# Performance work log

Hardware: AMD Instinct MI355X
Metric: run time of the kernel (lower is better)

## Reference

```python
import jax, jax.numpy as jnp
import numpy as np
import math

DIM = 1024
NUM_HEADS = 16
HEAD_DIM = DIM // NUM_HEADS  # 64
BATCH = 4
SEQ = 4096


def setup_inputs() -> dict:
    key = jax.random.key(0)
    ks = jax.random.split(key, 10)
    s = 1.0 / math.sqrt(DIM)
    return {
        "x": jax.random.normal(ks[0], (BATCH, SEQ, DIM), dtype=jnp.float32),
        "Wq": jax.random.normal(ks[1], (DIM, DIM), dtype=jnp.float32) * s,
        "bq": jax.random.normal(ks[2], (DIM,), dtype=jnp.float32) * 0.01,
        "Wk": jax.random.normal(ks[3], (DIM, DIM), dtype=jnp.float32) * s,
        "bk": jax.random.normal(ks[4], (DIM,), dtype=jnp.float32) * 0.01,
        "Wv": jax.random.normal(ks[5], (DIM, DIM), dtype=jnp.float32) * s,
        "bv": jax.random.normal(ks[6], (DIM,), dtype=jnp.float32) * 0.01,
        "Wo": jax.random.normal(ks[7], (DIM, DIM), dtype=jnp.float32) * s,
        "bo": jax.random.normal(ks[8], (DIM,), dtype=jnp.float32) * 0.01,
        # Performer random projection buffer: randn * 0.4, [head_dim, feature_map_size]
        "R": jax.random.normal(ks[9], (HEAD_DIM, HEAD_DIM), dtype=jnp.float32) * 0.4,
    }


def _feature_map(x, R):
    # x: [b, h, n, d]; matches torch: x scaled first, then norm of scaled x
    x = x / math.sqrt(HEAD_DIM)
    proj = jnp.einsum("bhnd,dm->bhnm", x, R)
    sq_norm = jnp.sum(x * x, axis=-1, keepdims=True)  # ||x||^2
    return jnp.exp(proj - 0.5 * sq_norm)


def reference(x, Wq, bq, Wk, bk, Wv, bv, Wo, bo, R):
    b, n, _ = x.shape
    h, d = NUM_HEADS, HEAD_DIM

    def split_heads(t):
        return t.reshape(b, n, h, d).transpose(0, 2, 1, 3)  # [b,h,n,d]

    q = split_heads(x @ Wq.T + bq)
    k = split_heads(x @ Wk.T + bk)
    v = split_heads(x @ Wv.T + bv)

    q_prime = _feature_map(q, R)  # [b,h,n,m]
    k_prime = _feature_map(k, R)  # [b,h,n,m]

    kv = jnp.einsum("bhnd,bhne->bhde", k_prime, v)          # [b,h,m,d]
    z = 1.0 / (jnp.sum(q_prime, axis=-1) + 1e-8)            # [b,h,n]
    out = jnp.einsum("bhnd,bhde,bhn->bhne", q_prime, kv, z)  # [b,h,n,d]

    out = out.transpose(0, 2, 1, 3).reshape(b, n, DIM)
    return out @ Wo.T + bo
```

## Files before the change

### kernel.cpp

```cpp
#include <hip/hip_runtime.h>
#include <math.h>

#define DIM 1024
#define NH 16
#define HD 64
#define BATCH 4
#define SEQ 4096
#define NTOK (BATCH*SEQ)

typedef float f32x4 __attribute__((ext_vector_type(4)));
typedef short bf16x8 __attribute__((ext_vector_type(8)));

#define GLOAD_LDS16(gp, lp)                                                    \
  __builtin_amdgcn_global_load_lds(                                            \
      (const __attribute__((address_space(1))) unsigned int*)(gp),             \
      (__attribute__((address_space(3))) unsigned int*)(lp), 16, 0, 0)

__device__ __forceinline__ unsigned short f2bf(float f) {
  unsigned u = __float_as_uint(f);
  unsigned r = (u + 0x7fffu + ((u >> 16) & 1u)) >> 16;
  return (unsigned short)r;
}
__device__ __forceinline__ float bf2f(unsigned short s) {
  return __uint_as_float((unsigned)s << 16);
}

template <int NT_N, int OUT_BF16>
__global__ __launch_bounds__(512, 2) void gemm256(
    const unsigned short* __restrict__ A,
    const unsigned short* __restrict__ B,
    const float* __restrict__ b0, const float* __restrict__ b1,
    const float* __restrict__ b2,
    void* __restrict__ C0, void* __restrict__ C1, void* __restrict__ C2)
{
    __shared__ unsigned short SA[4][8192];
    __shared__ unsigned short SB[4][8192];
    const int t    = threadIdx.x;
    const int lane = t & 63;
    const int w    = t >> 6;

    const int cpx = gridDim.x >> 3;
    const int swz = (blockIdx.x & 7) * cpx + (blockIdx.x >> 3);
    const int mi  = swz / NT_N;
    const int ni  = swz % NT_N;
    const int m0  = mi * 256;
    const int n0g = ni * 256;

    const int wm = (w >> 2) * 128;
    const int wn = (w & 3) * 64;

    const int srow = t >> 2;
    const int sseg = ((t & 3) ^ ((t >> 3) & 3)) * 8;
    const unsigned short* Ag = A + (size_t)(m0 + srow) * 1024 + sseg;
    const unsigned short* Bg = B + (size_t)(n0g + srow) * 1024 + sseg;
    const int ldst = w * 512;

    const int fr = lane & 15;
    const int fq = ((lane >> 4) ^ ((fr >> 1) & 3)) * 8;

    const unsigned abase = (unsigned)(size_t)
        (__attribute__((address_space(3))) unsigned short*)&SA[0][0]
        + (unsigned)(((wm + fr) * 32 + fq) * 2);
    const unsigned bbase = (unsigned)(size_t)
        (__attribute__((address_space(3))) unsigned short*)&SB[0][0]
        + (unsigned)(((wn + fr) * 32 + fq) * 2);

    f32x4 acc[8][4] = {};
    bf16x8 a1[4], a2[4], bb[2][4];

#define STGA(k, j)                                                            \
  GLOAD_LDS16(Ag + (size_t)(j) * 131072 + (size_t)(k) * 32,                   \
              &SA[(k) & 3][(j) * 4096 + ldst])
#define STGB(k, j)                                                            \
  GLOAD_LDS16(Bg + (size_t)(j) * 131072 + (size_t)(k) * 32,                   \
              &SB[(k) & 3][(j) * 4096 + ldst])
#define DSR(dst, base, imm)                                                   \
  asm volatile("ds_read_b128 %0, %1 offset:%2"                                \
               : "=v"(dst) : "v"(base), "i"(imm))
#define VMW_(N) asm volatile("s_waitcnt vmcnt(" #N ")" ::: "memory")
#define VMW(N) VMW_(N)
#define LGKM0                                                                 \
  asm volatile("s_waitcnt lgkmcnt(0)" ::: "memory");                          \
  __builtin_amdgcn_sched_barrier(0)
#define BARRIER                                                               \
  __builtin_amdgcn_s_barrier();                                               \
  __builtin_amdgcn_sched_barrier(0)

#define BODY(h, VM, DOSTG, DORD)                                              \
  {                                                                           \
    LGKM0;                                                                    \
    _Pragma("unroll")                                                         \
    for (int mf = 0; mf < 4; ++mf)                                            \
      DSR(a2[mf], abase, ((h) & 3) * 16384 + 4096 + mf * 1024);               \
    if (DOSTG) {                                                              \
      STGA((h) + 3, 0); STGA((h) + 3, 1);                                     \
      STGB((h) + 3, 0); STGB((h) + 3, 1);                                     \
    }                                                                         \
    __builtin_amdgcn_s_setprio(1);                                            \
    _Pragma("unroll")                                                         \
    for (int mf = 0; mf < 4; ++mf)                                            \
      _Pragma("unroll")                                                       \
      for (int nf = 0; nf < 4; ++nf)                                          \
        acc[mf][nf] = __builtin_amdgcn_mfma_f32_16x16x32_bf16(                \
            a1[mf], bb[(h) & 1][nf], acc[mf][nf], 0, 0, 0);                   \
    __builtin_amdgcn_s_setprio(0);                                            \
    VMW(VM);                                                                  \
    BARRIER;                                                                  \
    LGKM0;                                                                    \
    if (DORD) {                                                               \
      _Pragma("unroll")                                                       \
      for (int nf = 0; nf < 4; ++nf)                                          \
        DSR(bb[((h) + 1) & 1][nf], bbase,                                     \
            (((h) + 1) & 3) * 16384 + nf * 1024);                             \
      _Pragma("unroll")                                                       \
      for (int mf = 0; mf < 4; ++mf)                                          \
        DSR(a1[mf], abase, (((h) + 1) & 3) * 16384 + mf * 1024);              \
    }                                                                         \
    __builtin_amdgcn_s_setprio(1);                                            \
    _Pragma("unroll")                                                         \
    for (int mf = 0; mf < 4; ++mf)                                            \
      _Pragma("unroll")                                                       \
      for (int nf = 0; nf < 4; ++nf)                                          \
        acc[4 + mf][nf] = __builtin_amdgcn_mfma_f32_16x16x32_bf16(            \
            a2[mf], bb[(h) & 1][nf], acc[4 + mf][nf], 0, 0, 0);               \
    __builtin_amdgcn_s_setprio(0);                                            \
    BARRIER;                                                                  \
  }

    STGA(0, 0); STGA(0, 1); STGB(0, 0); STGB(0, 1);
    STGA(1, 0); STGA(1, 1); STGB(1, 0); STGB(1, 1);
    STGA(2, 0); STGA(2, 1); STGB(2, 0); STGB(2, 1);
    VMW(8);
    BARRIER;
#pragma unroll
    for (int nf = 0; nf < 4; ++nf)
        DSR(bb[0][nf], bbase, nf * 1024);
#pragma unroll
    for (int mf = 0; mf < 4; ++mf)
        DSR(a1[mf], abase, mf * 1024);

    BODY(0, 8, 1, 1)  BODY(1, 8, 1, 1)  BODY(2, 8, 1, 1)  BODY(3, 8, 1, 1)
    BODY(4, 8, 1, 1)  BODY(5, 8, 1, 1)  BODY(6, 8, 1, 1)  BODY(7, 8, 1, 1)
    BODY(8, 8, 1, 1)  BODY(9, 8, 1, 1)  BODY(10, 8, 1, 1) BODY(11, 8, 1, 1)
    BODY(12, 8, 1, 1) BODY(13, 8, 1, 1) BODY(14, 8, 1, 1) BODY(15, 8, 1, 1)
    BODY(16, 8, 1, 1) BODY(17, 8, 1, 1) BODY(18, 8, 1, 1) BODY(19, 8, 1, 1)
    BODY(20, 8, 1, 1) BODY(21, 8, 1, 1) BODY(22, 8, 1, 1) BODY(23, 8, 1, 1)
    BODY(24, 8, 1, 1) BODY(25, 8, 1, 1) BODY(26, 8, 1, 1) BODY(27, 8, 1, 1)
    BODY(28, 8, 1, 1) BODY(29, 4, 0, 1) BODY(30, 0, 0, 1) BODY(31, 0, 0, 0)

#undef BODY
#undef BARRIER
#undef LGKM0
#undef VMW
#undef VMW_
#undef DSR
#undef STGB
#undef STGA

    const int mat = ni >> 2;
    const float* bias = (mat == 0) ? b0 : (mat == 1) ? b1 : b2;
    void* Cp = (mat == 0) ? C0 : (mat == 1) ? C1 : C2;
    const int n0 = (ni & 3) * 256;

    const int col = lane & 15;
    const int rq  = (lane >> 4) * 4;
#pragma unroll
    for (int nf = 0; nf < 4; ++nf) {
        int cbase = n0 + wn + nf * 16 + col;
        float bv = bias[cbase];
#pragma unroll
        for (int mf = 0; mf < 8; ++mf) {
            int rbase = m0 + wm + (mf >> 2) * 64 + (mf & 3) * 16 + rq;
#pragma unroll
            for (int r = 0; r < 4; ++r) {
                float val = acc[mf][nf][r] + bv;
                size_t idx = (size_t)(rbase + r) * 1024 + cbase;
                if (OUT_BF16)
                    ((unsigned short*)Cp)[idx] = f2bf(val);
                else
                    ((float*)Cp)[idx] = val;
            }
        }
    }
}

__global__ __launch_bounds__(256) void cast_bf16(
    const float* __restrict__ src, unsigned short* __restrict__ dst, int n)
{
    int i = (blockIdx.x * 256 + threadIdx.x) * 4;
    if (i >= n) return;
    float4 v = *(const float4*)&src[i];
    ushort2 lo = {f2bf(v.x), f2bf(v.y)};
    ushort2 hi = {f2bf(v.z), f2bf(v.w)};
    *(ushort2*)&dst[i] = lo;
    *(ushort2*)&dst[i + 2] = hi;
}

__global__ __launch_bounds__(256) void cast_bf16_w4(
    const float* __restrict__ s0, const float* __restrict__ s1,
    const float* __restrict__ s2, const float* __restrict__ s3,
    unsigned short* __restrict__ d0, unsigned short* __restrict__ d1,
    unsigned short* __restrict__ d2, unsigned short* __restrict__ d3)
{
    const float* s = (blockIdx.y == 0) ? s0 : (blockIdx.y == 1) ? s1
                    : (blockIdx.y == 2) ? s2 : s3;
    unsigned short* d = (blockIdx.y == 0) ? d0 : (blockIdx.y == 1) ? d1
                       : (blockIdx.y == 2) ? d2 : d3;
    int i = (blockIdx.x * 256 + threadIdx.x) * 4;
    float4 v = *(const float4*)&s[i];
    ushort2 lo = {f2bf(v.x), f2bf(v.y)};
    ushort2 hi = {f2bf(v.z), f2bf(v.w)};
    *(ushort2*)&d[i] = lo;
    *(ushort2*)&d[i + 2] = hi;
}

__global__ __launch_bounds__(256) void featmap_mfma(
    unsigned short* __restrict__ buf, const float* __restrict__ R)
{
    __shared__ unsigned short Rt[64 * 72];
    const int t = threadIdx.x;
    for (int i = t; i < 4096; i += 256) {
        int n = i >> 6, k = i & 63;
        Rt[n * 72 + k] = f2bf(R[k * 64 + n]);
    }
    __syncthreads();

    const int lane = t & 63;
    const int w = t >> 6;
    const size_t rowbase = (size_t)blockIdx.x * 256 + w * 64;
    const int fr = lane & 15;
    const int fq = (lane >> 4) * 8;

    f32x4 acc[4][4] = {};
    float sqacc[4] = {0.f, 0.f, 0.f, 0.f};

#pragma unroll
    for (int ks = 0; ks < 2; ks++) {
        bf16x8 bfr[4];
#pragma unroll
        for (int nt = 0; nt < 4; nt++)
            bfr[nt] = *(const bf16x8*)&Rt[(nt * 16 + fr) * 72 + ks * 32 + fq];
#pragma unroll
        for (int mt = 0; mt < 4; mt++) {
            bf16x8 a = *(const bf16x8*)
                &buf[(rowbase + mt * 16 + fr) * 64 + ks * 32 + fq];
#pragma unroll
            for (int j = 0; j < 8; j++) {
                float v = bf2f((unsigned short)a[j]);
                sqacc[mt] = fmaf(v, v, sqacc[mt]);
            }
#pragma unroll
            for (int nt = 0; nt < 4; nt++)
                acc[mt][nt] = __builtin_amdgcn_mfma_f32_16x16x32_bf16(
                    a, bfr[nt], acc[mt][nt], 0, 0, 0);
        }
    }
#pragma unroll
    for (int mt = 0; mt < 4; mt++) {
        sqacc[mt] += __shfl_xor(sqacc[mt], 16);
        sqacc[mt] += __shfl_xor(sqacc[mt], 32);
    }

    const int col = lane & 15;
    const int rq  = (lane >> 4) * 4;
#pragma unroll
    for (int mt = 0; mt < 4; mt++) {
#pragma unroll
        for (int r = 0; r < 4; r++) {
            float s = __shfl(sqacc[mt], rq + r);
            size_t row = rowbase + mt * 16 + rq + r;
#pragma unroll
            for (int nt = 0; nt < 4; nt++) {
                float val = acc[mt][nt][r] * 0.125f - s * 0.0078125f;
                buf[row * 64 + nt * 16 + col] = f2bf(__expf(val));
            }
        }
    }
}

__global__ __launch_bounds__(256) void kv_accum(
    const unsigned short* __restrict__ kp, const unsigned short* __restrict__ vp,
    float* __restrict__ kv)
{
    __shared__ float Ks[16][68];
    __shared__ float Vs[16][68];
    const int chunk = blockIdx.x;
    const int h = blockIdx.y;
    const int b = blockIdx.z;
    const int t = threadIdx.x;
    const int tx = t & 15, ty = t >> 4;
    float c[4][4] = {};
    const int nbase = b * SEQ + chunk * 512;
    const int nl = t >> 4, seg = t & 15;
    for (int n0 = 0; n0 < 512; n0 += 16) {
        size_t gaddr = (size_t)(nbase + n0 + nl) * DIM + h * 64 + seg * 4;
        ushort4 kq = *(const ushort4*)&kp[gaddr];
        ushort4 vq = *(const ushort4*)&vp[gaddr];
        Ks[nl][seg * 4 + 0] = bf2f(kq.x); Ks[nl][seg * 4 + 1] = bf2f(kq.y);
        Ks[nl][seg * 4 + 2] = bf2f(kq.z); Ks[nl][seg * 4 + 3] = bf2f(kq.w);
        Vs[nl][seg * 4 + 0] = bf2f(vq.x); Vs[nl][seg * 4 + 1] = bf2f(vq.y);
        Vs[nl][seg * 4 + 2] = bf2f(vq.z); Vs[nl][seg * 4 + 3] = bf2f(vq.w);
        __syncthreads();
#pragma unroll
        for (int nn = 0; nn < 16; nn++) {
            float4 a = *(const float4*)&Ks[nn][ty * 4];
            float4 bq = *(const float4*)&Vs[nn][tx * 4];
            float aa[4] = {a.x, a.y, a.z, a.w};
            float bb[4] = {bq.x, bq.y, bq.z, bq.w};
#pragma unroll
            for (int i = 0; i < 4; i++)
#pragma unroll
                for (int j = 0; j < 4; j++)
                    c[i][j] += aa[i] * bb[j];
        }
        __syncthreads();
    }
    float* dst = &kv[(size_t)(b * NH + h) * 64 * 64];
#pragma unroll
    for (int i = 0; i < 4; i++)
#pragma unroll
        for (int j = 0; j < 4; j++)
            atomicAdd(&dst[(ty * 4 + i) * 64 + tx * 4 + j], c[i][j]);
}

__global__ __launch_bounds__(256) void attn_out_mfma(
    const unsigned short* __restrict__ qp, const float* __restrict__ kv,
    unsigned short* __restrict__ ob)
{
    __shared__ unsigned short kvT[64 * 72];
    const int t = threadIdx.x;
    const int bh = blockIdx.y;
    const int b = bh >> 4, h = bh & 15;
    const float* kvp = &kv[(size_t)bh * 4096];
    for (int i = t; i < 4096; i += 256) {
        int m = i >> 6, e = i & 63;
        kvT[e * 72 + m] = f2bf(kvp[i]);
    }
    __syncthreads();

    const int lane = t & 63;
    const int w = t >> 6;
    const int rowInSeq = blockIdx.x * 256 + w * 64;
    const int fr = lane & 15;
    const int fq = (lane >> 4) * 8;

    f32x4 acc[4][4] = {};
    float rsum[4] = {0.f, 0.f, 0.f, 0.f};

#pragma unroll
    for (int ks = 0; ks < 2; ks++) {
        bf16x8 bfr[4];
#pragma unroll
        for (int nt = 0; nt < 4; nt++)
            bfr[nt] = *(const bf16x8*)&kvT[(nt * 16 + fr) * 72 + ks * 32 + fq];
#pragma unroll
        for (int mt = 0; mt < 4; mt++) {
            size_t n = (size_t)(b * SEQ + rowInSeq + mt * 16 + fr);
            bf16x8 a = *(const bf16x8*)&qp[n * DIM + h * 64 + ks * 32 + fq];
#pragma unroll
            for (int j = 0; j < 8; j++)
                rsum[mt] += bf2f((unsigned short)a[j]);
#pragma unroll
            for (int nt = 0; nt < 4; nt++)
                acc[mt][nt] = __builtin_amdgcn_mfma_f32_16x16x32_bf16(
                    a, bfr[nt], acc[mt][nt], 0, 0, 0);
        }
    }
#pragma unroll
    for (int mt = 0; mt < 4; mt++) {
        rsum[mt] += __shfl_xor(rsum[mt], 16);
        rsum[mt] += __shfl_xor(rsum[mt], 32);
    }

    const int col = lane & 15;
    const int rq  = (lane >> 4) * 4;
#pragma unroll
    for (int mt = 0; mt < 4; mt++) {
#pragma unroll
        for (int r = 0; r < 4; r++) {
            float s = __shfl(rsum[mt], rq + r);
            float z = 1.f / (s + 1e-8f);
            size_t n = (size_t)(b * SEQ + rowInSeq + mt * 16 + rq + r);
#pragma unroll
            for (int nt = 0; nt < 4; nt++)
                ob[n * DIM + h * 64 + nt * 16 + col] = f2bf(acc[mt][nt][r] * z);
        }
    }
}

extern "C" void kernel_launch(void* const* d_in, const int* in_sizes, int n_in,
                              void* d_out, int out_size, void* d_ws, size_t ws_size,
                              hipStream_t stream) {
    const float* x  = (const float*)d_in[0];
    const float* Wq = (const float*)d_in[1];
    const float* bq = (const float*)d_in[2];
    const float* Wk = (const float*)d_in[3];
    const float* bk = (const float*)d_in[4];
    const float* Wv = (const float*)d_in[5];
    const float* bv = (const float*)d_in[6];
    const float* Wo = (const float*)d_in[7];
    const float* bo = (const float*)d_in[8];
    const float* R  = (const float*)d_in[9];
    float* out = (float*)d_out;

    char* p = (char*)d_ws;
    unsigned short* xb = (unsigned short*)p; p += (size_t)NTOK * DIM * 2;
    unsigned short* qb = (unsigned short*)p; p += (size_t)NTOK * DIM * 2;
    unsigned short* kb = (unsigned short*)p; p += (size_t)NTOK * DIM * 2;
    unsigned short* vb = (unsigned short*)p; p += (size_t)NTOK * DIM * 2;
    float* kvb = (float*)p;                  p += (size_t)BATCH * NH * HD * HD * 4;
    unsigned short* wqkv = (unsigned short*)p; p += (size_t)3 * DIM * DIM * 2;
    unsigned short* wob  = (unsigned short*)p; p += (size_t)DIM * DIM * 2;

    hipMemsetAsync(kvb, 0, (size_t)BATCH * NH * HD * HD * sizeof(float), stream);

    cast_bf16<<<NTOK * DIM / (256 * 4), 256, 0, stream>>>(x, xb, NTOK * DIM);
    cast_bf16_w4<<<dim3(DIM * DIM / (256 * 4), 4), 256, 0, stream>>>(
        Wq, Wk, Wv, Wo,
        wqkv, wqkv + (size_t)DIM * DIM, wqkv + (size_t)2 * DIM * DIM, wob);

    gemm256<12, 1><<<768, 512, 0, stream>>>(
        xb, wqkv, bq, bk, bv, qb, kb, vb);

    featmap_mfma<<<2 * NTOK * NH / 256, 256, 0, stream>>>(qb, R);

    kv_accum<<<dim3(8, NH, BATCH), 256, 0, stream>>>(kb, vb, kvb);

    attn_out_mfma<<<dim3(SEQ / 256, BATCH * NH), 256, 0, stream>>>(qb, kvb, xb);

    gemm256<4, 0><<<256, 512, 0, stream>>>(
        xb, wob, bo, bo, bo, out, out, out);
}
```

Measured before the change: 419.0 us.

## Fuse Performer feature map into QKV GEMM epilogue and merge cast kernels

The QKV projection GEMM now applies the Performer feature map (projection by R, squared norm, exp) directly in its epilogue for the Q and K outputs. It stages the bias-added tile in LDS, runs small MFMAs against a transposed bf16 copy of R, and writes the exponentiated features instead of raw Q/K. This removes the separate featmap kernel and its read-modify-write pass over Q and K. The input and weight cast kernels are also merged into one launch. In exchange the epilogue gets heavier, with more LDS traffic and register pressure, and the squared norm is now taken from fp32 values rather than bf16-rounded ones.

```diff
diff --git a/kernel.cpp b/kernel.cpp
--- a/kernel.cpp
+++ b/kernel.cpp
@@ -25,16 +25,16 @@
   return __uint_as_float((unsigned)s << 16);
 }
 
-template <int NT_N, int OUT_BF16>
+template <int NT_N, int OUT_BF16, int FUSE_FM>
 __global__ __launch_bounds__(512, 2) void gemm256(
     const unsigned short* __restrict__ A,
     const unsigned short* __restrict__ B,
     const float* __restrict__ b0, const float* __restrict__ b1,
     const float* __restrict__ b2,
-    void* __restrict__ C0, void* __restrict__ C1, void* __restrict__ C2)
+    void* __restrict__ C0, void* __restrict__ C1, void* __restrict__ C2,
+    const float* __restrict__ Rg)
 {
-    __shared__ unsigned short SA[4][8192];
-    __shared__ unsigned short SB[4][8192];
+    __shared__ __align__(16) unsigned short LDSU[65536];
     const int t    = threadIdx.x;
     const int lane = t & 63;
     const int w    = t >> 6;
@@ -58,22 +58,20 @@
     const int fr = lane & 15;
     const int fq = ((lane >> 4) ^ ((fr >> 1) & 3)) * 8;
 
-    const unsigned abase = (unsigned)(size_t)
-        (__attribute__((address_space(3))) unsigned short*)&SA[0][0]
-        + (unsigned)(((wm + fr) * 32 + fq) * 2);
-    const unsigned bbase = (unsigned)(size_t)
-        (__attribute__((address_space(3))) unsigned short*)&SB[0][0]
-        + (unsigned)(((wn + fr) * 32 + fq) * 2);
+    const unsigned lbase = (unsigned)(size_t)
+        (__attribute__((address_space(3))) unsigned short*)&LDSU[0];
+    const unsigned abase = lbase + (unsigned)(((wm + fr) * 32 + fq) * 2);
+    const unsigned bbase = lbase + 65536u + (unsigned)(((wn + fr) * 32 + fq) * 2);
 
     f32x4 acc[8][4] = {};
     bf16x8 a1[4], a2[4], bb[2][4];
 
 #define STGA(k, j)                                                            \
   GLOAD_LDS16(Ag + (size_t)(j) * 131072 + (size_t)(k) * 32,                   \
-              &SA[(k) & 3][(j) * 4096 + ldst])
+              &LDSU[((k) & 3) * 8192 + (j) * 4096 + ldst])
 #define STGB(k, j)                                                            \
   GLOAD_LDS16(Bg + (size_t)(j) * 131072 + (size_t)(k) * 32,                   \
-              &SB[(k) & 3][(j) * 4096 + ldst])
+              &LDSU[32768 + ((k) & 3) * 8192 + (j) * 4096 + ldst])
 #define DSR(dst, base, imm)                                                   \
   asm volatile("ds_read_b128 %0, %1 offset:%2"                                \
                : "=v"(dst) : "v"(base), "i"(imm))
@@ -161,121 +159,126 @@
     const float* bias = (mat == 0) ? b0 : (mat == 1) ? b1 : b2;
     void* Cp = (mat == 0) ? C0 : (mat == 1) ? C1 : C2;
     const int n0 = (ni & 3) * 256;
-
     const int col = lane & 15;
     const int rq  = (lane >> 4) * 4;
-#pragma unroll
-    for (int nf = 0; nf < 4; ++nf) {
-        int cbase = n0 + wn + nf * 16 + col;
-        float bv = bias[cbase];
-#pragma unroll
-        for (int mf = 0; mf < 8; ++mf) {
-            int rbase = m0 + wm + (mf >> 2) * 64 + (mf & 3) * 16 + rq;
-#pragma unroll
-            for (int r = 0; r < 4; ++r) {
-                float val = acc[mf][nf][r] + bv;
-                size_t idx = (size_t)(rbase + r) * 1024 + cbase;
-                if (OUT_BF16)
-                    ((unsigned short*)Cp)[idx] = f2bf(val);
-                else
-                    ((float*)Cp)[idx] = val;
+
+    if (FUSE_FM && mat < 2) {
+        for (int i = t; i < 4096; i += 512) {
+            int n2 = i >> 6, k2 = i & 63;
+            LDSU[36864 + n2 * 72 + k2] = f2bf(Rg[k2 * 64 + n2]);
+        }
+        asm volatile("s_waitcnt lgkmcnt(0)" ::: "memory");
+        __builtin_amdgcn_s_barrier();
+
+        unsigned short* wlds = &LDSU[w * 4608];
+        const int fq0 = (lane >> 4) * 8;
+        const int hcol0 = n0 + wn;
+        float bv4[4];
+#pragma unroll
+        for (int nf = 0; nf < 4; ++nf) bv4[nf] = bias[hcol0 + nf * 16 + col];
+
+#pragma unroll
+        for (int p = 0; p < 2; ++p) {
+            float s4[4][4];
+#pragma unroll
+            for (int mfl = 0; mfl < 4; ++mfl)
+#pragma unroll
+                for (int r = 0; r < 4; ++r) s4[mfl][r] = 0.f;
+#pragma unroll
+            for (int mfl = 0; mfl < 4; ++mfl)
+#pragma unroll
+                for (int nf = 0; nf < 4; ++nf)
+#pragma unroll
+                    for (int r = 0; r < 4; ++r) {
+                        float val = acc[p * 4 + mfl][nf][r] + bv4[nf];
+                        s4[mfl][r] = fmaf(val, val, s4[mfl][r]);
+                        wlds[(mfl * 16 + rq + r) * 72 + nf * 16 + col] = f2bf(val);
+                    }
+#pragma unroll
+            for (int mfl = 0; mfl < 4; ++mfl)
+#pragma unroll
+                for (int r = 0; r < 4; ++r) {
+                    s4[mfl][r] += __shfl_xor(s4[mfl][r], 1);
+                    s4[mfl][r] += __shfl_xor(s4[mfl][r], 2);
+                    s4[mfl][r] += __shfl_xor(s4[mfl][r], 4);
+                    s4[mfl][r] += __shfl_xor(s4[mfl][r], 8);
+                }
+            f32x4 pr[4][4] = {};
+#pragma unroll
+            for (int ks = 0; ks < 2; ++ks) {
+                bf16x8 bfr[4];
+#pragma unroll
+                for (int nt = 0; nt < 4; ++nt)
+                    bfr[nt] = *(const bf16x8*)
+                        &LDSU[36864 + (nt * 16 + fr) * 72 + ks * 32 + fq0];
+#pragma unroll
+                for (int mfl = 0; mfl < 4; ++mfl) {
+                    bf16x8 af = *(const bf16x8*)
+                        &wlds[(mfl * 16 + fr) * 72 + ks * 32 + fq0];
+#pragma unroll
+                    for (int nt = 0; nt < 4; ++nt)
+                        pr[mfl][nt] = __builtin_amdgcn_mfma_f32_16x16x32_bf16(
+                            af, bfr[nt], pr[mfl][nt], 0, 0, 0);
+                }
             }
-        }
-    }
-}
-
-__global__ __launch_bounds__(256) void cast_bf16(
-    const float* __restrict__ src, unsigned short* __restrict__ dst, int n)
+#pragma unroll
+            for (int mfl = 0; mfl < 4; ++mfl)
+#pragma unroll
+                for (int r = 0; r < 4; ++r) {
+                    float ss = s4[mfl][r] * 0.0078125f;
+                    size_t row = (size_t)(m0 + wm + p * 64 + mfl * 16 + rq + r);
+#pragma unroll
+                    for (int nt = 0; nt < 4; ++nt) {
+                        float e = __expf(pr[mfl][nt][r] * 0.125f - ss);
+                        ((unsigned short*)Cp)[row * 1024 + hcol0 + nt * 16 + col]
+                            = f2bf(e);
+                    }
+                }
+            if (p == 0) asm volatile("s_waitcnt lgkmcnt(0)" ::: "memory");
+        }
+    } else {
+#pragma unroll
+        for (int nf = 0; nf < 4; ++nf) {
+            int cbase = n0 + wn + nf * 16 + col;
+            float bv = bias[cbase];
+#pragma unroll
+            for (int mf = 0; mf < 8; ++mf) {
+                int rbase = m0 + wm + (mf >> 2) * 64 + (mf & 3) * 16 + rq;
+#pragma unroll
+                for (int r = 0; r < 4; ++r) {
+                    float val = acc[mf][nf][r] + bv;
+                    size_t idx = (size_t)(rbase + r) * 1024 + cbase;
+                    if (OUT_BF16)
+                        ((unsigned short*)Cp)[idx] = f2bf(val);
+                    else
+                        ((float*)Cp)[idx] = val;
+                }
+            }
+        }
+    }
+}
+
+__global__ __launch_bounds__(256) void cast_all(
+    const float* __restrict__ x,  const float* __restrict__ Wq,
+    const float* __restrict__ Wk, const float* __restrict__ Wv,
+    const float* __restrict__ Wo,
+    unsigned short* __restrict__ xb, unsigned short* __restrict__ wqkv,
+    unsigned short* __restrict__ wob)
 {
-    int i = (blockIdx.x * 256 + threadIdx.x) * 4;
-    if (i >= n) return;
-    float4 v = *(const float4*)&src[i];
+    const size_t NX = (size_t)NTOK * DIM;
+    const size_t NW = (size_t)DIM * DIM;
+    size_t i = ((size_t)blockIdx.x * 256 + threadIdx.x) * 4;
+    const float* s; unsigned short* d; size_t off;
+    if (i < NX)               { s = x;  d = xb;             off = i; }
+    else if (i < NX + NW)     { s = Wq; d = wqkv;           off = i - NX; }
+    else if (i < NX + 2 * NW) { s = Wk; d = wqkv + NW;      off = i - NX - NW; }
+    else if (i < NX + 3 * NW) { s = Wv; d = wqkv + 2 * NW;  off = i - NX - 2 * NW; }
+    else                      { s = Wo; d = wob;            off = i - NX - 3 * NW; }
+    float4 v = *(const float4*)&s[off];
     ushort2 lo = {f2bf(v.x), f2bf(v.y)};
     ushort2 hi = {f2bf(v.z), f2bf(v.w)};
-    *(ushort2*)&dst[i] = lo;
-    *(ushort2*)&dst[i + 2] = hi;
-}
-
-__global__ __launch_bounds__(256) void cast_bf16_w4(
-    const float* __restrict__ s0, const float* __restrict__ s1,
-    const float* __restrict__ s2, const float* __restrict__ s3,
-    unsigned short* __restrict__ d0, unsigned short* __restrict__ d1,
-    unsigned short* __restrict__ d2, unsigned short* __restrict__ d3)
-{
-    const float* s = (blockIdx.y == 0) ? s0 : (blockIdx.y == 1) ? s1
-                    : (blockIdx.y == 2) ? s2 : s3;
-    unsigned short* d = (blockIdx.y == 0) ? d0 : (blockIdx.y == 1) ? d1
-                       : (blockIdx.y == 2) ? d2 : d3;
-    int i = (blockIdx.x * 256 + threadIdx.x) * 4;
-    float4 v = *(const float4*)&s[i];
-    ushort2 lo = {f2bf(v.x), f2bf(v.y)};
-    ushort2 hi = {f2bf(v.z), f2bf(v.w)};
-    *(ushort2*)&d[i] = lo;
-    *(ushort2*)&d[i + 2] = hi;
-}
-
-__global__ __launch_bounds__(256) void featmap_mfma(
-    unsigned short* __restrict__ buf, const float* __restrict__ R)
-{
-    __shared__ unsigned short Rt[64 * 72];
-    const int t = threadIdx.x;
-    for (int i = t; i < 4096; i += 256) {
-        int n = i >> 6, k = i & 63;
-        Rt[n * 72 + k] = f2bf(R[k * 64 + n]);
-    }
-    __syncthreads();
-
-    const int lane = t & 63;
-    const int w = t >> 6;
-    const size_t rowbase = (size_t)blockIdx.x * 256 + w * 64;
-    const int fr = lane & 15;
-    const int fq = (lane >> 4) * 8;
-
-    f32x4 acc[4][4] = {};
-    float sqacc[4] = {0.f, 0.f, 0.f, 0.f};
-
-#pragma unroll
-    for (int ks = 0; ks < 2; ks++) {
-        bf16x8 bfr[4];
-#pragma unroll
-        for (int nt = 0; nt < 4; nt++)
-            bfr[nt] = *(const bf16x8*)&Rt[(nt * 16 + fr) * 72 + ks * 32 + fq];
-#pragma unroll
-        for (int mt = 0; mt < 4; mt++) {
-            bf16x8 a = *(const bf16x8*)
-                &buf[(rowbase + mt * 16 + fr) * 64 + ks * 32 + fq];
-#pragma unroll
-            for (int j = 0; j < 8; j++) {
-                float v = bf2f((unsigned short)a[j]);
-                sqacc[mt] = fmaf(v, v, sqacc[mt]);
-            }
-#pragma unroll
-            for (int nt = 0; nt < 4; nt++)
-                acc[mt][nt] = __builtin_amdgcn_mfma_f32_16x16x32_bf16(
-                    a, bfr[nt], acc[mt][nt], 0, 0, 0);
-        }
-    }
-#pragma unroll
-    for (int mt = 0; mt < 4; mt++) {
-        sqacc[mt] += __shfl_xor(sqacc[mt], 16);
-        sqacc[mt] += __shfl_xor(sqacc[mt], 32);
-    }
-
-    const int col = lane & 15;
-    const int rq  = (lane >> 4) * 4;
-#pragma unroll
-    for (int mt = 0; mt < 4; mt++) {
-#pragma unroll
-        for (int r = 0; r < 4; r++) {
-            float s = __shfl(sqacc[mt], rq + r);
-            size_t row = rowbase + mt * 16 + rq + r;
-#pragma unroll
-            for (int nt = 0; nt < 4; nt++) {
-                float val = acc[mt][nt][r] * 0.125f - s * 0.0078125f;
-                buf[row * 64 + nt * 16 + col] = f2bf(__expf(val));
-            }
-        }
-    }
+    *(ushort2*)&d[off] = lo;
+    *(ushort2*)&d[off + 2] = hi;
 }
 
 __global__ __launch_bounds__(256) void kv_accum(
@@ -414,20 +417,16 @@
 
     hipMemsetAsync(kvb, 0, (size_t)BATCH * NH * HD * HD * sizeof(float), stream);
 
-    cast_bf16<<<NTOK * DIM / (256 * 4), 256, 0, stream>>>(x, xb, NTOK * DIM);
-    cast_bf16_w4<<<dim3(DIM * DIM / (256 * 4), 4), 256, 0, stream>>>(
-        Wq, Wk, Wv, Wo,
-        wqkv, wqkv + (size_t)DIM * DIM, wqkv + (size_t)2 * DIM * DIM, wob);
-
-    gemm256<12, 1><<<768, 512, 0, stream>>>(
-        xb, wqkv, bq, bk, bv, qb, kb, vb);
-
-    featmap_mfma<<<2 * NTOK * NH / 256, 256, 0, stream>>>(qb, R);
+    cast_all<<<(NTOK * DIM + 4 * DIM * DIM) / (256 * 4), 256, 0, stream>>>(
+        x, Wq, Wk, Wv, Wo, xb, wqkv, wob);
+
+    gemm256<12, 1, 1><<<768, 512, 0, stream>>>(
+        xb, wqkv, bq, bk, bv, qb, kb, vb, R);
 
     kv_accum<<<dim3(8, NH, BATCH), 256, 0, stream>>>(kb, vb, kvb);
 
     attn_out_mfma<<<dim3(SEQ / 256, BATCH * NH), 256, 0, stream>>>(qb, kvb, xb);
 
-    gemm256<4, 0><<<256, 512, 0, stream>>>(
-        xb, wob, bo, bo, bo, out, out, out);
-}
+    gemm256<4, 0, 0><<<256, 512, 0, stream>>>(
+        xb, wob, bo, bo, bo, out, out, out, nullptr);
+}
```

Result: faster. 380.7 us (-9.1%).
